# Kernel tuning notes

Hardware: AMD Instinct MI355X
Metric: run time of the kernel (lower is better)

Reference implementation:

```python
import math
import jax, jax.numpy as jnp
import numpy as np

B, S, D = 4, 4096, 1024

def setup_inputs() -> dict:
    key = jax.random.key(0)
    ks = jax.random.split(key, 4)
    scale = 1.0 / math.sqrt(D)
    return {
        "x": jax.random.normal(ks[0], (B, S, D), dtype=jnp.float32),
        "Wq": jax.random.normal(ks[1], (D, D), dtype=jnp.float32) * scale,
        "bq": jnp.zeros((D,), dtype=jnp.float32),
        "Wk": jax.random.normal(ks[2], (D, D), dtype=jnp.float32) * scale,
        "bk": jnp.zeros((D,), dtype=jnp.float32),
        "Wv": jax.random.normal(ks[3], (D, D), dtype=jnp.float32) * scale,
        "bv": jnp.zeros((D,), dtype=jnp.float32),
    }

def reference(x, Wq, bq, Wk, bk, Wv, bv):
    # Linear layers (torch nn.Linear: x @ W.T + b)
    Q = jnp.einsum('bsd,ed->bse', x, Wq) + bq  # [B,S,D]
    K = jnp.einsum('bsd,ed->bse', x, Wk) + bk
    V = jnp.einsum('bsd,ed->bse', x, Wv) + bv
    # Full (non-flash) attention, scaled by sqrt(hidden_dim) as in source
    scores = jnp.einsum('bqd,bkd->bqk', Q, K) / jnp.sqrt(jnp.float32(Q.shape[-1]))
    attn = jax.nn.softmax(scores, axis=-1)  # [B,S,S]
    return jnp.einsum('bqk,bkd->bqd', attn, V)
```

## Files before the change

### kernel.cpp

```cpp
#include <hip/hip_runtime.h>
#include <hip/hip_bf16.h>
#include <stdint.h>


typedef __attribute__((ext_vector_type(4))) float f32x4;
typedef __attribute__((ext_vector_type(8))) short s16x8;
typedef __attribute__((ext_vector_type(4))) unsigned short u16x4;
typedef unsigned int u32;
typedef unsigned short u16;

__device__ __forceinline__ u16 f2b(float f) {
  u32 u = __float_as_uint(f);
  u = (u + 0x7FFFu + ((u >> 16) & 1u)) >> 16;
  return (u16)u;
}
__device__ __forceinline__ float b2f(u16 h) {
  return __uint_as_float(((u32)h) << 16);
}

__device__ __forceinline__ void gload_lds16(const void* g, void* l) {
  __builtin_amdgcn_global_load_lds(
      (const __attribute__((address_space(1))) void*)(const void*)g,
      (__attribute__((address_space(3))) void*)(void*)l, 16, 0, 0);
}

#define BARRIER() asm volatile("s_barrier" ::: "memory")
#define WAITLGKM0() asm volatile("s_waitcnt lgkmcnt(0)" ::: "memory")
#define WAITVM(N) asm volatile("s_waitcnt vmcnt(" #N ")" ::: "memory")

__global__ __launch_bounds__(256) void k_cvt(const float* __restrict__ in,
                                             u16* __restrict__ out, int n4) {
  int i = blockIdx.x * 256 + threadIdx.x;
  if (i >= n4) return;
  f32x4 f = ((const f32x4*)in)[i];
  u16x4 h;
#pragma unroll
  for (int j = 0; j < 4; ++j) h[j] = f2b(f[j]);
  ((u16x4*)out)[i] = h;
}

template <int MODE>
__global__ __launch_bounds__(512)
void k_gemm256(const u16* __restrict__ A, const u16* __restrict__ B, int lda,
               int ldb, int K, const float* __restrict__ bias,
               const float* __restrict__ biasB, void* __restrict__ Cv, int ldc,
               float scale, size_t az, size_t bz, size_t czb,
               float* __restrict__ part) {
  extern __shared__ __align__(16) u16 lds[];

  A += (size_t)blockIdx.z * az;
  B += (size_t)blockIdx.z * bz;
  char* C = (char*)Cv + (size_t)blockIdx.z * czb;
  const float* bi = (MODE == 0 && blockIdx.z != 0) ? biasB : bias;

  const int gx = gridDim.x;
  const int nwg = gx * gridDim.y;
  const int bid = blockIdx.y * gx + blockIdx.x;
  const int q = nwg >> 3, r = nwg & 7;
  const int xcd = bid & 7, idx = bid >> 3;
  const int tile = (xcd < r ? xcd * (q + 1) : r * (q + 1) + (xcd - r) * q) + idx;
  const int m0 = (tile / gx) * 256;
  const int n0 = (tile % gx) * 256;

  const int tid = threadIdx.x;
  const int lane = tid & 63;
  const int wid = tid >> 6;
  const int wm = wid >> 2;
  const int wn = wid & 3;

  const int srow = lane >> 3;
  const int gcol = (((lane & 7) ^ srow) << 3);
  const int rA = lane & 15;
  const int kq = (lane >> 4) << 3;
  const int xr = (lane & 7) << 3;

#define STAGE_A(h, kt, b)                                                    \
  do {                                                                       \
    _Pragma("unroll") for (int j = 0; j < 2; ++j)                            \
        gload_lds16(A + (size_t)(m0 + (h)*128 + j * 64 + wid * 8 + srow) *   \
                            lda + (kt)*64 + gcol,                            \
                    &lds[(b)*32768 + (h)*8192 + j * 4096 + wid * 512]);      \
  } while (0)
#define STAGE_B(h, kt, b)                                                    \
  do {                                                                       \
    _Pragma("unroll") for (int j = 0; j < 2; ++j)                            \
        gload_lds16(B + (size_t)(n0 + (h)*128 + j * 64 + wid * 8 + srow) *   \
                            ldb + (kt)*64 + gcol,                            \
                    &lds[(b)*32768 + 16384 + (h)*8192 + j * 4096 +           \
                         wid * 512]);                                        \
  } while (0)
#define RD_A(dst, b, sub)                                                    \
  do {                                                                       \
    _Pragma("unroll") for (int mi = 0; mi < 4; ++mi)                         \
        _Pragma("unroll") for (int ks = 0; ks < 2; ++ks)                     \
            dst[mi][ks] = *(const s16x8*)&lds[(b)*32768 +                    \
                (wm * 128 + (sub) + mi * 16 + rA) * 64 +                     \
                ((ks * 32 + kq) ^ xr)];                                      \
  } while (0)
#define RD_B(dst, b, sub)                                                    \
  do {                                                                       \
    _Pragma("unroll") for (int ni = 0; ni < 2; ++ni)                         \
        _Pragma("unroll") for (int ks = 0; ks < 2; ++ks)                     \
            dst[ni][ks] = *(const s16x8*)&lds[(b)*32768 + 16384 +            \
                (wn * 64 + (sub) + ni * 16 + rA) * 64 +                      \
                ((ks * 32 + kq) ^ xr)];                                      \
  } while (0)
#define MM(AF, BF, MO, NO)                                                   \
  do {                                                                       \
    _Pragma("unroll") for (int mi = 0; mi < 4; ++mi)                         \
        _Pragma("unroll") for (int ni = 0; ni < 2; ++ni)                     \
            _Pragma("unroll") for (int ks = 0; ks < 2; ++ks)                 \
                acc[(MO) + mi][(NO) + ni] =                                  \
                    __builtin_amdgcn_mfma_f32_16x16x32_bf16(                 \
                        AF[mi][ks], BF[ni][ks], acc[(MO) + mi][(NO) + ni],   \
                        0, 0, 0);                                            \
  } while (0)

  f32x4 acc[8][4] = {};
  const int NT = K >> 6;

  STAGE_A(0, 0, 0);
  STAGE_A(1, 0, 0);
  STAGE_B(0, 0, 0);
  STAGE_B(1, 0, 0);
  if (NT > 1) {
    STAGE_A(0, 1, 1);
    STAGE_A(1, 1, 1);
    STAGE_B(0, 1, 1);
    STAGE_B(1, 1, 1);
    WAITVM(8);
  } else {
    WAITVM(0);
  }
  BARRIER();

  s16x8 af0[4][2], af1[4][2], bf0[2][2], bf1[2][2];
  for (int t = 0; t < NT; ++t) {
    const int b = t & 1;
    RD_A(af0, b, 0);
    RD_B(bf0, b, 0);
    WAITLGKM0();
    __builtin_amdgcn_s_setprio(1);
    MM(af0, bf0, 0, 0);
    __builtin_amdgcn_s_setprio(0);
    BARRIER();
    RD_A(af1, b, 64);
    WAITLGKM0();
    __builtin_amdgcn_s_setprio(1);
    MM(af1, bf0, 4, 0);
    __builtin_amdgcn_s_setprio(0);
    BARRIER();
    RD_B(bf1, b, 32);
    if (t + 2 < NT) {
      STAGE_A(0, t + 2, b);
      STAGE_A(1, t + 2, b);
    }
    WAITLGKM0();
    __builtin_amdgcn_s_setprio(1);
    MM(af0, bf1, 0, 2);
    __builtin_amdgcn_s_setprio(0);
    BARRIER();
    if (t + 2 < NT) {
      STAGE_B(0, t + 2, b);
      STAGE_B(1, t + 2, b);
    }
    __builtin_amdgcn_s_setprio(1);
    MM(af1, bf1, 4, 2);
    __builtin_amdgcn_s_setprio(0);
    if (t + 2 < NT) {
      WAITVM(8);
    } else {
      WAITVM(0);
    }
    BARRIER();
  }

  float* fl = (float*)lds;
  float* rinv = fl + 16640;
  const int l15 = lane & 15;
  const int r4 = (lane >> 4) * 4;
  f32x4 bcol4 = {0.f, 0.f, 0.f, 0.f};
  if (MODE == 0) bcol4 = *(const f32x4*)&bi[n0 + lane * 4];
  if (MODE == 3) {
    if (tid < 256) {
      const float* pr = &part[((size_t)blockIdx.z * 4096 + m0 + tid) * 16];
      float s = 0.f;
#pragma unroll
      for (int j = 0; j < 4; ++j) {
        f32x4 t4 = *(const f32x4*)&pr[j * 4];
        s += (t4[0] + t4[1]) + (t4[2] + t4[3]);
      }
      rinv[tid] = 1.0f / s;
    }
  }
#pragma unroll
  for (int c = 0; c < 4; ++c) {
    __syncthreads();
    if (wm == (c >> 1)) {
      const int mibase = (c & 1) * 4;
#pragma unroll
      for (int mi = 0; mi < 4; ++mi) {
#pragma unroll
        for (int nj = 0; nj < 4; ++nj) {
          const int col = wn * 64 + nj * 16 + l15;
          const int rbase = mi * 16 + r4;
#pragma unroll
          for (int rr = 0; rr < 4; ++rr) {
            float v = acc[mibase + mi][nj][rr];
            if (MODE == 2) v = __expf(v * scale);
            fl[(rbase + rr) * 260 + col] = v;
          }
        }
      }
    }
    __syncthreads();
#pragma unroll
    for (int p = 0; p < 8; ++p) {
      const int rl = p * 8 + wid;
      const int rowg = m0 + c * 64 + rl;
      f32x4 v = *(const f32x4*)&fl[rl * 260 + lane * 4];
      if (MODE == 0) {
#pragma unroll
        for (int j = 0; j < 4; ++j) v[j] += bcol4[j];
        u16x4 h;
#pragma unroll
        for (int j = 0; j < 4; ++j) h[j] = f2b(v[j]);
        ((u16x4*)((u16*)C + (size_t)rowg * ldc + n0))[lane] = h;
      } else if (MODE == 1) {
        const float br = bi[rowg];
        u16x4 h;
#pragma unroll
        for (int j = 0; j < 4; ++j) h[j] = f2b(v[j] + br);
        ((u16x4*)((u16*)C + (size_t)rowg * ldc + n0))[lane] = h;
      } else if (MODE == 2) {
        u16x4 h;
#pragma unroll
        for (int j = 0; j < 4; ++j) h[j] = f2b(v[j]);
        ((u16x4*)((u16*)C + (size_t)rowg * ldc + n0))[lane] = h;
      } else {
        const float iv = rinv[c * 64 + rl];
#pragma unroll
        for (int j = 0; j < 4; ++j) v[j] *= iv;
        ((f32x4*)((float*)C + (size_t)rowg * ldc + n0))[lane] = v;
      }
    }
    if (MODE == 2) {
      const int row8 = tid >> 3;
      const int seg = tid & 7;
      const float* rp = &fl[row8 * 260 + seg * 32];
      f32x4 s4 = {0.f, 0.f, 0.f, 0.f};
#pragma unroll
      for (int j = 0; j < 8; ++j) {
        f32x4 t4 = *(const f32x4*)&rp[j * 4];
#pragma unroll
        for (int d = 0; d < 4; ++d) s4[d] += t4[d];
      }
      float s = (s4[0] + s4[1]) + (s4[2] + s4[3]);
      s += __shfl_xor(s, 1, 64);
      s += __shfl_xor(s, 2, 64);
      s += __shfl_xor(s, 4, 64);
      if (seg == 0)
        part[((size_t)blockIdx.z * 4096 + m0 + c * 64 + row8) * 16 +
             (n0 >> 8)] = s;
    }
  }
#undef STAGE_A
#undef STAGE_B
#undef RD_A
#undef RD_B
#undef MM
}

extern "C" void kernel_launch(void* const* d_in, const int* in_sizes, int n_in,
                              void* d_out, int out_size, void* d_ws,
                              size_t ws_size, hipStream_t stream) {
  const float* x = (const float*)d_in[0];
  const float* Wq = (const float*)d_in[1];
  const float* bq = (const float*)d_in[2];
  const float* Wk = (const float*)d_in[3];
  const float* bk = (const float*)d_in[4];
  const float* Wv = (const float*)d_in[5];
  const float* bv = (const float*)d_in[6];
  float* out = (float*)d_out;
  char* ws = (char*)d_ws;

  const size_t MB = 1ull << 20;
  u16* Qb = (u16*)(ws + 0 * MB);
  u16* Kb = (u16*)(ws + 32 * MB);
  u16* VtAll = (u16*)(ws + 64 * MB);
  u16* Xb = (u16*)(ws + 96 * MB);
  u16* Sc = (u16*)(ws + 96 * MB);
  u16* Wqb = (u16*)(ws + 224 * MB);
  u16* Wkb = Wqb + 1048576;
  u16* Wvb = Wqb + 2097152;
  float* part = (float*)(ws + 231 * MB);

  hipFuncSetAttribute((const void*)k_gemm256<0>,
                      hipFuncAttributeMaxDynamicSharedMemorySize, 131072);
  hipFuncSetAttribute((const void*)k_gemm256<1>,
                      hipFuncAttributeMaxDynamicSharedMemorySize, 131072);
  hipFuncSetAttribute((const void*)k_gemm256<2>,
                      hipFuncAttributeMaxDynamicSharedMemorySize, 131072);
  hipFuncSetAttribute((const void*)k_gemm256<3>,
                      hipFuncAttributeMaxDynamicSharedMemorySize, 131072);

  k_cvt<<<16384, 256, 0, stream>>>(x, Xb, 4194304);
  k_cvt<<<1024, 256, 0, stream>>>(Wq, Wqb, 262144);
  k_cvt<<<1024, 256, 0, stream>>>(Wk, Wkb, 262144);
  k_cvt<<<1024, 256, 0, stream>>>(Wv, Wvb, 262144);

  dim3 blk(512);
  const size_t LDSB = 131072;
  k_gemm256<0><<<dim3(4, 64, 2), blk, LDSB, stream>>>(
      Xb, Wqb, 1024, 1024, 1024, bq, bk, Qb, 1024, 1.f, 0, 1048576,
      (size_t)32 * MB, nullptr);
  k_gemm256<1><<<dim3(64, 4, 1), blk, LDSB, stream>>>(
      Wvb, Xb, 1024, 1024, 1024, bv, nullptr, VtAll, 16384, 1.f, 0, 0, 0,
      nullptr);
  k_gemm256<2><<<dim3(16, 16, 4), blk, LDSB, stream>>>(
      Qb, Kb, 1024, 1024, 1024, nullptr, nullptr, Sc, 4096, 0.03125f, 4194304,
      4194304, (size_t)4096 * 4096 * 2, part);
  k_gemm256<3><<<dim3(4, 16, 4), blk, LDSB, stream>>>(
      Sc, VtAll, 4096, 16384, 4096, nullptr, nullptr, out, 1024, 1.f, 16777216,
      4096, (size_t)4096 * 1024 * 4, part);
}
```

Measured before the change: 413.3 us.

## Restructure GEMM main loop: load all B fragments once, halve barriers

The GEMM inner loop now reads all four B fragment groups from LDS at once and runs two larger MFMA phases instead of four, dropping two of the four barriers per K-step. A tiles are prefetched one step ahead into the other buffer, while B tiles stay two steps ahead, and the vmcnt waits are adjusted to match. The aim is to cut synchronization and LDS-read overhead between MFMA bursts. In exchange it uses more fragment registers, which may lower occupancy, and A loads now have less lead time to hide latency.

```diff
diff --git a/kernel.cpp b/kernel.cpp
--- a/kernel.cpp
+++ b/kernel.cpp
@@ -97,22 +97,22 @@
                 (wm * 128 + (sub) + mi * 16 + rA) * 64 +                     \
                 ((ks * 32 + kq) ^ xr)];                                      \
   } while (0)
-#define RD_B(dst, b, sub)                                                    \
-  do {                                                                       \
-    _Pragma("unroll") for (int ni = 0; ni < 2; ++ni)                         \
+#define RD_BALL(dst, b)                                                      \
+  do {                                                                       \
+    _Pragma("unroll") for (int nj = 0; nj < 4; ++nj)                         \
         _Pragma("unroll") for (int ks = 0; ks < 2; ++ks)                     \
-            dst[ni][ks] = *(const s16x8*)&lds[(b)*32768 + 16384 +            \
-                (wn * 64 + (sub) + ni * 16 + rA) * 64 +                      \
+            dst[nj][ks] = *(const s16x8*)&lds[(b)*32768 + 16384 +            \
+                (wn * 64 + nj * 16 + rA) * 64 +                              \
                 ((ks * 32 + kq) ^ xr)];                                      \
   } while (0)
-#define MM(AF, BF, MO, NO)                                                   \
+#define MM2(AF, BF, MO)                                                      \
   do {                                                                       \
     _Pragma("unroll") for (int mi = 0; mi < 4; ++mi)                         \
-        _Pragma("unroll") for (int ni = 0; ni < 2; ++ni)                     \
+        _Pragma("unroll") for (int nj = 0; nj < 4; ++nj)                     \
             _Pragma("unroll") for (int ks = 0; ks < 2; ++ks)                 \
-                acc[(MO) + mi][(NO) + ni] =                                  \
+                acc[(MO) + mi][nj] =                                         \
                     __builtin_amdgcn_mfma_f32_16x16x32_bf16(                 \
-                        AF[mi][ks], BF[ni][ks], acc[(MO) + mi][(NO) + ni],   \
+                        AF[mi][ks], BF[nj][ks], acc[(MO) + mi][nj],          \
                         0, 0, 0);                                            \
   } while (0)
 
@@ -124,51 +124,39 @@
   STAGE_B(0, 0, 0);
   STAGE_B(1, 0, 0);
   if (NT > 1) {
-    STAGE_A(0, 1, 1);
-    STAGE_A(1, 1, 1);
     STAGE_B(0, 1, 1);
     STAGE_B(1, 1, 1);
-    WAITVM(8);
+    WAITVM(4);
   } else {
     WAITVM(0);
   }
   BARRIER();
 
-  s16x8 af0[4][2], af1[4][2], bf0[2][2], bf1[2][2];
+  s16x8 af0[4][2], af1[4][2], bf[4][2];
   for (int t = 0; t < NT; ++t) {
     const int b = t & 1;
     RD_A(af0, b, 0);
-    RD_B(bf0, b, 0);
+    RD_BALL(bf, b);
+    if (t + 1 < NT) {
+      STAGE_A(0, t + 1, b ^ 1);
+      STAGE_A(1, t + 1, b ^ 1);
+    }
     WAITLGKM0();
     __builtin_amdgcn_s_setprio(1);
-    MM(af0, bf0, 0, 0);
+    MM2(af0, bf, 0);
     __builtin_amdgcn_s_setprio(0);
     BARRIER();
     RD_A(af1, b, 64);
-    WAITLGKM0();
-    __builtin_amdgcn_s_setprio(1);
-    MM(af1, bf0, 4, 0);
-    __builtin_amdgcn_s_setprio(0);
-    BARRIER();
-    RD_B(bf1, b, 32);
-    if (t + 2 < NT) {
-      STAGE_A(0, t + 2, b);
-      STAGE_A(1, t + 2, b);
-    }
-    WAITLGKM0();
-    __builtin_amdgcn_s_setprio(1);
-    MM(af0, bf1, 0, 2);
-    __builtin_amdgcn_s_setprio(0);
-    BARRIER();
     if (t + 2 < NT) {
       STAGE_B(0, t + 2, b);
       STAGE_B(1, t + 2, b);
     }
+    WAITLGKM0();
     __builtin_amdgcn_s_setprio(1);
-    MM(af1, bf1, 4, 2);
+    MM2(af1, bf, 4);
     __builtin_amdgcn_s_setprio(0);
     if (t + 2 < NT) {
-      WAITVM(8);
+      WAITVM(4);
     } else {
       WAITVM(0);
     }
@@ -267,8 +255,8 @@
 #undef STAGE_A
 #undef STAGE_B
 #undef RD_A
-#undef RD_B
-#undef MM
+#undef RD_BALL
+#undef MM2
 }
 
 extern "C" void kernel_launch(void* const* d_in, const int* in_sizes, int n_in,
```

After: 407.4 us. About the same (-1.4%).
